# Performance work log

Measured on AMD Instinct MI355X. Metric: run time of the kernel, lower is better.

The kernel has to match this reference:

```python
import jax, jax.numpy as jnp
import numpy as np

D_MODEL = 1024
N_HEADS = 16
NUM_EXPERTS = 8
GATE_HIDDEN = 128
B, T = 4, 2048


def setup_inputs() -> dict:
    key = jax.random.key(0)
    ks = jax.random.split(key, 14)
    s = 0.02
    d, e, gh = D_MODEL, NUM_EXPERTS, GATE_HIDDEN
    return {
        "hidden_states": jax.random.normal(ks[0], (B, T, d), jnp.float32),
        # torch Linear weights are [out_features, in_features]
        "Wq": jax.random.normal(ks[1], (e, d, d), jnp.float32) * s,
        "bq": jax.random.normal(ks[2], (e, d), jnp.float32) * s,
        "Wk": jax.random.normal(ks[3], (e, d, d), jnp.float32) * s,
        "bk": jax.random.normal(ks[4], (e, d), jnp.float32) * s,
        "Wv": jax.random.normal(ks[5], (e, d, d), jnp.float32) * s,
        "bv": jax.random.normal(ks[6], (e, d), jnp.float32) * s,
        "Wg1": jax.random.normal(ks[7], (gh, d), jnp.float32) * s,
        "bg1": jax.random.normal(ks[8], (gh,), jnp.float32) * s,
        "Wg2": jax.random.normal(ks[9], (e, gh), jnp.float32) * s,
        "bg2": jax.random.normal(ks[10], (e,), jnp.float32) * s,
        "Wo": jax.random.normal(ks[11], (d, d), jnp.float32) * s,
        "bo": jax.random.normal(ks[12], (d,), jnp.float32) * s,
    }


def reference(hidden_states, Wq, bq, Wk, bk, Wv, bv, Wg1, bg1, Wg2, bg2, Wo, bo):
    Bb, Tt, C = hidden_states.shape
    H = N_HEADS
    Dh = C // H

    # Per-sample gating over mean-pooled sequence
    pooled = hidden_states.mean(axis=1)                        # [B, C]
    gate_h = jax.nn.relu(pooled @ Wg1.T + bg1)                 # [B, 128]
    gw = jax.nn.softmax(gate_h @ Wg2.T + bg2, axis=-1)         # [B, E]

    # Since gating weights are per-batch scalars, sum_e w_e * (x W_e^T + b_e)
    # == x (sum_e w_e W_e)^T + sum_e w_e b_e  — same math, one GEMM per sample.
    def proj(We, be):
        W_eff = jnp.einsum('be,eoi->boi', gw, We)              # [B, C, C]
        b_eff = gw @ be                                        # [B, C]
        y = jnp.einsum('bti,boi->bto', hidden_states, W_eff) + b_eff[:, None, :]
        return y.reshape(Bb, Tt, H, Dh).transpose(0, 2, 1, 3)  # [B, H, T, Dh]

    q = proj(Wq, bq)
    k = proj(Wk, bk)
    v = proj(Wv, bv)

    scores = jnp.einsum('bhtd,bhsd->bhts', q, k) / (Dh ** 0.5)
    attn = jax.nn.softmax(scores, axis=-1)                     # dropout is inference identity
    out = jnp.einsum('bhts,bhsd->bhtd', attn, v)
    out = out.transpose(0, 2, 1, 3).reshape(Bb, Tt, C)
    return out @ Wo.T + bo
```

## Files before the change

kernel.cpp:

```cpp
#include <hip/hip_runtime.h>

#define B_ 4
#define T_ 2048
#define C_ 1024
#define H_ 16
#define DH_ 64
#define E_ 8
#define GH_ 128

typedef unsigned short bf16_t;
typedef __attribute__((ext_vector_type(8))) __bf16 bf16x8;
typedef __attribute__((ext_vector_type(2))) __bf16 bf16x2;
typedef __attribute__((ext_vector_type(4))) float floatx4;

#if __has_builtin(__builtin_amdgcn_exp2f)
#define EXP2F(x) __builtin_amdgcn_exp2f(x)
#else
#define EXP2F(x) exp2f(x)
#endif

__device__ __forceinline__ bf16_t f2bf(float f) {
  unsigned int u = __builtin_bit_cast(unsigned int, f);
  u += 0x7fffu + ((u >> 16) & 1u);
  return (bf16_t)(u >> 16);
}
__device__ __forceinline__ void async16(const void* g, void* l) {
  __builtin_amdgcn_global_load_lds(
      (const __attribute__((address_space(1))) unsigned int*)g,
      (__attribute__((address_space(3))) unsigned int*)l, 16, 0, 0);
}

__global__ void cvt_kernel(const float* __restrict__ src, bf16_t* __restrict__ dst) {
  int i = (blockIdx.x * 256 + threadIdx.x) * 4;
  float4 v = *(const float4*)(src + i);
  bf16_t o4[4] = {f2bf(v.x), f2bf(v.y), f2bf(v.z), f2bf(v.w)};
  *(uint2*)(dst + i) = *(const uint2*)o4;
}

__global__ void pool_kernel(const float* __restrict__ x, float* __restrict__ partial) {
  int bz = blockIdx.x;
  int b = bz >> 4;
  int r0 = (bz & 15) * 128;
  int t = threadIdx.x;
  float a0 = 0.f, a1 = 0.f, a2 = 0.f, a3 = 0.f;
  const float* xb = x + (size_t)b * T_ * C_ + (size_t)r0 * C_;
  for (int r = 0; r < 128; ++r) {
    const float* row = xb + (size_t)r * C_;
    a0 += row[t]; a1 += row[t + 256]; a2 += row[t + 512]; a3 += row[t + 768];
  }
  float* p = partial + (size_t)bz * C_;
  p[t] = a0; p[t + 256] = a1; p[t + 512] = a2; p[t + 768] = a3;
}

__global__ void gate_kernel(const float* __restrict__ partial,
                            const float* __restrict__ Wg1, const float* __restrict__ bg1,
                            const float* __restrict__ Wg2, const float* __restrict__ bg2,
                            const float* __restrict__ bq, const float* __restrict__ bk,
                            const float* __restrict__ bv,
                            float* __restrict__ gw, float* __restrict__ beff) {
  int b = blockIdx.x;
  int t = threadIdx.x;
  __shared__ float spool[C_];
  __shared__ float sh[GH_];
  __shared__ float sgw[E_];
  for (int i = t; i < C_; i += GH_) {
    float s = 0.f;
    for (int j = 0; j < 16; ++j) s += partial[(size_t)(b * 16 + j) * C_ + i];
    spool[i] = s * (1.0f / T_);
  }
  __syncthreads();
  {
    float acc = 0.f;
    const float* wr = Wg1 + (size_t)t * C_;
    for (int i = 0; i < C_; i += 4) {
      float4 w = *(const float4*)(wr + i);
      acc += spool[i] * w.x + spool[i + 1] * w.y + spool[i + 2] * w.z + spool[i + 3] * w.w;
    }
    acc += bg1[t];
    sh[t] = fmaxf(acc, 0.0f);
  }
  __syncthreads();
  if (t < E_) {
    float acc = 0.f;
    const float* wr = Wg2 + t * GH_;
    for (int j = 0; j < GH_; ++j) acc += sh[j] * wr[j];
    sgw[t] = acc + bg2[t];
  }
  __syncthreads();
  if (t == 0) {
    float mx = sgw[0];
    for (int e = 1; e < E_; ++e) mx = fmaxf(mx, sgw[e]);
    float s = 0.f, ex[E_];
    for (int e = 0; e < E_; ++e) { ex[e] = __expf(sgw[e] - mx); s += ex[e]; }
    float inv = 1.0f / s;
    for (int e = 0; e < E_; ++e) { sgw[e] = ex[e] * inv; gw[b * E_ + e] = sgw[e]; }
  }
  __syncthreads();
  for (int o = t; o < C_; o += GH_) {
    float aq = 0.f, ak = 0.f, av = 0.f;
    #pragma unroll
    for (int e = 0; e < E_; ++e) {
      float w = sgw[e];
      aq += w * bq[e * C_ + o];
      ak += w * bk[e * C_ + o];
      av += w * bv[e * C_ + o];
    }
    beff[(0 * B_ + b) * C_ + o] = aq;
    beff[(1 * B_ + b) * C_ + o] = ak;
    beff[(2 * B_ + b) * C_ + o] = av;
  }
}

__global__ void combine_kernel(const float* __restrict__ Wq, const float* __restrict__ Wk,
                               const float* __restrict__ Wv, const float* __restrict__ gw,
                               bf16_t* __restrict__ Weff) {
  int g = blockIdx.x * 256 + threadIdx.x;
  int ig = (g & 127) * 8;
  int o = (g >> 7) & 1023;
  int p = g >> 17;
  const float* W = (p == 0) ? Wq : (p == 1) ? Wk : Wv;
  const float* src = W + (size_t)o * C_ + ig;
  float acc[B_][8];
  #pragma unroll
  for (int b = 0; b < B_; ++b)
    #pragma unroll
    for (int j = 0; j < 8; ++j) acc[b][j] = 0.f;
  #pragma unroll
  for (int e = 0; e < E_; ++e) {
    float4 lo = *(const float4*)(src + (size_t)e * C_ * C_);
    float4 hi = *(const float4*)(src + (size_t)e * C_ * C_ + 4);
    float w8[8] = {lo.x, lo.y, lo.z, lo.w, hi.x, hi.y, hi.z, hi.w};
    #pragma unroll
    for (int b = 0; b < B_; ++b) {
      float wgt = gw[b * E_ + e];
      #pragma unroll
      for (int j = 0; j < 8; ++j) acc[b][j] += wgt * w8[j];
    }
  }
  #pragma unroll
  for (int b = 0; b < B_; ++b) {
    bf16_t out8[8];
    #pragma unroll
    for (int j = 0; j < 8; ++j) out8[j] = f2bf(acc[b][j]);
    *(uint4*)(Weff + ((size_t)p * B_ + b) * C_ * C_ + (size_t)o * C_ + ig) = *(const uint4*)out8;
  }
}

template <int MODE>
__global__ __launch_bounds__(256) void gemm128(const bf16_t* __restrict__ X,
                                               const bf16_t* __restrict__ W,
                                               const float* __restrict__ bias,
                                               bf16_t* __restrict__ Yb,
                                               float* __restrict__ Yf) {
  if (MODE == 0) {
    int z = blockIdx.z;
    X += (size_t)(z & 3) * (T_ * C_);
    W += (size_t)z * (C_ * C_);
    bias += (size_t)z * C_;
    Yb += (size_t)z * (T_ * C_);
  }
  const int n0 = blockIdx.x * 128;
  const int m0 = blockIdx.y * 128;

  __shared__ __align__(16) bf16_t As[128][64];
  __shared__ __align__(16) bf16_t Bs[128][64];

  const int tid = threadIdx.x;
  const int wave = tid >> 6;
  const int lane = tid & 63;
  const int quad = lane >> 4;
  const int l16 = lane & 15;
  const int wm = (wave & 1) * 64;
  const int wn = (wave >> 1) * 64;

  floatx4 acc[4][4];
  #pragma unroll
  for (int i = 0; i < 4; ++i)
    #pragma unroll
    for (int j = 0; j < 4; ++j) { floatx4 zz = {0.f, 0.f, 0.f, 0.f}; acc[i][j] = zz; }

  const int ar = tid >> 3;
  const int ac = (tid & 7) * 8;
  const bf16_t* Xp = X + (size_t)(m0 + ar) * C_ + ac;
  const bf16_t* Wp = W + (size_t)(n0 + ar) * C_ + ac;

  for (int k0 = 0; k0 < C_; k0 += 64) {
    __syncthreads();
    #pragma unroll
    for (int s = 0; s < 4; ++s) {
      async16(Xp + (size_t)(s * 32) * C_ + k0, &As[ar + s * 32][ac]);
      async16(Wp + (size_t)(s * 32) * C_ + k0, &Bs[ar + s * 32][ac]);
    }
    __syncthreads();
    #pragma unroll
    for (int kk = 0; kk < 64; kk += 32) {
      bf16x8 af[4], bfr[4];
      #pragma unroll
      for (int i = 0; i < 4; ++i) {
        af[i] = *(const bf16x8*)(&As[wm + i * 16 + l16][kk + quad * 8]);
        bfr[i] = *(const bf16x8*)(&Bs[wn + i * 16 + l16][kk + quad * 8]);
      }
      #pragma unroll
      for (int mi = 0; mi < 4; ++mi)
        #pragma unroll
        for (int ni = 0; ni < 4; ++ni)
          acc[mi][ni] = __builtin_amdgcn_mfma_f32_16x16x32_bf16(af[mi], bfr[ni], acc[mi][ni], 0, 0, 0);
    }
  }

  #pragma unroll
  for (int mi = 0; mi < 4; ++mi) {
    #pragma unroll
    for (int ni = 0; ni < 4; ++ni) {
      const int n = n0 + wn + ni * 16 + l16;
      const float bv = bias[n];
      #pragma unroll
      for (int r = 0; r < 4; ++r) {
        const int m = m0 + wm + mi * 16 + quad * 4 + r;
        float v = acc[mi][ni][r] + bv;
        if (MODE == 0) Yb[((size_t)(n >> 6) * T_ + m) * DH_ + (n & 63)] = f2bf(v);
        else           Yf[(size_t)m * C_ + n] = v;
      }
    }
  }
}

__global__ void vtrans_kernel(const bf16_t* __restrict__ qkv, bf16_t* __restrict__ Vt) {
  const int kt = blockIdx.x;
  const int bh = blockIdx.y;
  const int b = bh >> 4, h = bh & 15;
  const bf16_t* src = qkv + (size_t)(8 + b) * T_ * C_ + (size_t)h * T_ * DH_ + (size_t)kt * 64 * DH_;
  __shared__ __align__(16) bf16_t L[64][64];
  const int t = threadIdx.x;
  const int r = t >> 2;
  const int c = (t & 3) * 16;
  const int sw = r & 48;
  *(uint4*)(&L[r][c ^ sw]) = *(const uint4*)(src + (size_t)r * DH_ + c);
  *(uint4*)(&L[r][(c ^ sw) + 8]) = *(const uint4*)(src + (size_t)r * DH_ + c + 8);
  __syncthreads();
  const int sw2 = c & 48;
  bf16_t tmp[16];
  #pragma unroll
  for (int j = 0; j < 16; ++j) tmp[j] = L[c + j][r ^ sw2];
  bf16_t* dst = Vt + (size_t)bh * DH_ * T_ + (size_t)r * T_ + (size_t)kt * 64 + c;
  *(uint4*)(dst) = *(const uint4*)(tmp);
  *(uint4*)(dst + 8) = *(const uint4*)(tmp + 8);
}

__global__ __launch_bounds__(512, 6) void attn_kernel(const bf16_t* __restrict__ qkv,
                                                      const bf16_t* __restrict__ Vt,
                                                      bf16_t* __restrict__ out) {
  const int bh = blockIdx.x;
  const int qt = blockIdx.y;
  const int b = bh >> 4, h = bh & 15;
  const __bf16* Q = (const __bf16*)(qkv + (size_t)b * T_ * C_ + (size_t)h * T_ * DH_);
  const bf16_t* Kp = qkv + (size_t)(4 + b) * T_ * C_ + (size_t)h * T_ * DH_;
  const bf16_t* Vtb = Vt + (size_t)bh * DH_ * T_;

  __shared__ __align__(16) bf16_t Ks[2][4096];
  __shared__ __align__(16) bf16_t Vs[2][4096];
  __shared__ __align__(16) __bf16 Ps[128][72];

  const int tid = threadIdx.x;
  const int wave = tid >> 6;
  const int lane = tid & 63;
  const int quad = lane >> 4;
  const int l16 = lane & 15;

  const float QSC = 0.125f * 1.44269504f;
  bf16x8 qb[2];
  {
    const __bf16* qrow = Q + (size_t)(qt * 128 + wave * 16 + l16) * DH_;
    #pragma unroll
    for (int kc = 0; kc < 2; ++kc) {
      union { bf16x8 v; __bf16 e[8]; } fr;
      #pragma unroll
      for (int j = 0; j < 8; ++j) fr.e[j] = (__bf16)((float)qrow[kc * 32 + quad * 8 + j] * QSC);
      qb[kc] = fr.v;
    }
  }

  int off_[2][4];
  #pragma unroll
  for (int kc = 0; kc < 2; ++kc) {
    #pragma unroll
    for (int i = 0; i < 4; ++i) {
      int row = i * 16 + l16;
      off_[kc][i] = ((row << 3) + (((kc << 2) + quad) ^ (row & 7))) * 8;
    }
  }
  __bf16* prow = &Ps[wave * 16 + l16][0];
  const bf16x8* paptr0 = (const bf16x8*)(prow + 0 * 32 + quad * 8);
  const bf16x8* paptr1 = (const bf16x8*)(prow + 1 * 32 + quad * 8);

  floatx4 oacc[4];
  #pragma unroll
  for (int di = 0; di < 4; ++di) { floatx4 zz = {0.f, 0.f, 0.f, 0.f}; oacc[di] = zz; }
  float lrun = 0.f;

  const int srow = tid >> 3;
  const int schk = (tid & 7) ^ (srow & 7);
  const bf16_t* kg = Kp + (size_t)srow * DH_ + schk * 8;
  const bf16_t* vg = Vtb + (size_t)srow * T_ + schk * 8;

#define STAGE(BUF) do {                                   \
    async16(kg, &Ks[BUF][tid * 8]);                       \
    async16(vg, &Vs[BUF][tid * 8]);                       \
    kg += 64 * DH_;                                       \
    vg += 64;                                             \
  } while (0)

#define WAITV(N) asm volatile("s_waitcnt vmcnt(" #N ")" ::: "memory")
#define BAR() __builtin_amdgcn_s_barrier()

#define COMPUTE(CUR) do {                                                            \
    floatx4 s_[4];                                                                   \
    _Pragma("unroll")                                                                \
    for (int ni = 0; ni < 4; ++ni) { floatx4 zz = {0.f, 0.f, 0.f, 0.f}; s_[ni] = zz; } \
    __builtin_amdgcn_s_setprio(1);                                                   \
    _Pragma("unroll")                                                                \
    for (int kc = 0; kc < 2; ++kc) {                                                 \
      _Pragma("unroll")                                                              \
      for (int ni = 0; ni < 4; ++ni) {                                               \
        bf16x8 ka = *(const bf16x8*)(&Ks[CUR][off_[kc][ni]]);                        \
        s_[ni] = __builtin_amdgcn_mfma_f32_16x16x32_bf16(ka, qb[kc], s_[ni], 0, 0, 0); \
      }                                                                              \
    }                                                                                \
    __builtin_amdgcn_s_setprio(0);                                                   \
    float lsum = 0.f;                                                                \
    _Pragma("unroll")                                                                \
    for (int ni = 0; ni < 4; ++ni) {                                                 \
      float p0 = EXP2F(s_[ni][0]);                                                   \
      float p1 = EXP2F(s_[ni][1]);                                                   \
      float p2 = EXP2F(s_[ni][2]);                                                   \
      float p3 = EXP2F(s_[ni][3]);                                                   \
      lsum += (p0 + p1) + (p2 + p3);                                                 \
      bf16x2 w0 = {(__bf16)p0, (__bf16)p1};                                          \
      bf16x2 w1 = {(__bf16)p2, (__bf16)p3};                                          \
      uint2 pk;                                                                      \
      pk.x = __builtin_bit_cast(unsigned int, w0);                                   \
      pk.y = __builtin_bit_cast(unsigned int, w1);                                   \
      *(uint2*)(prow + ni * 16 + quad * 4) = pk;                                     \
    }                                                                                \
    lsum += __shfl_xor(lsum, 16);                                                    \
    lsum += __shfl_xor(lsum, 32);                                                    \
    lrun += lsum;                                                                    \
    __builtin_amdgcn_s_setprio(1);                                                   \
    _Pragma("unroll")                                                                \
    for (int kc = 0; kc < 2; ++kc) {                                                 \
      bf16x8 pa = *(kc == 0 ? paptr0 : paptr1);                                      \
      _Pragma("unroll")                                                              \
      for (int di = 0; di < 4; ++di) {                                               \
        bf16x8 vb = *(const bf16x8*)(&Vs[CUR][off_[kc][di]]);                        \
        oacc[di] = __builtin_amdgcn_mfma_f32_16x16x32_bf16(pa, vb, oacc[di], 0, 0, 0); \
      }                                                                              \
    }                                                                                \
    __builtin_amdgcn_s_setprio(0);                                                   \
  } while (0)

  STAGE(0);
  #pragma unroll 1
  for (int kt = 0; kt < 30; kt += 2) {
    STAGE(1);
    WAITV(2);
    BAR();
    COMPUTE(0);
    BAR();
    STAGE(0);
    WAITV(2);
    BAR();
    COMPUTE(1);
    BAR();
  }
  STAGE(1);
  WAITV(2);
  BAR();
  COMPUTE(0);
  BAR();
  WAITV(0);
  BAR();
  COMPUTE(1);

#undef STAGE
#undef WAITV
#undef BAR
#undef COMPUTE

  float linv = 1.0f / lrun;
  #pragma unroll
  for (int r = 0; r < 4; ++r) {
    float li = __shfl(linv, quad * 20 + r);
    int m = qt * 128 + wave * 16 + quad * 4 + r;
    #pragma unroll
    for (int di = 0; di < 4; ++di) {
      int d = di * 16 + l16;
      out[(size_t)b * T_ * C_ + (size_t)m * C_ + h * DH_ + d] = f2bf(oacc[di][r] * li);
    }
  }
}

extern "C" void kernel_launch(void* const* d_in, const int* in_sizes, int n_in,
                              void* d_out, int out_size, void* d_ws, size_t ws_size,
                              hipStream_t stream) {
  (void)in_sizes; (void)n_in; (void)out_size; (void)ws_size;
  const float* x   = (const float*)d_in[0];
  const float* Wq  = (const float*)d_in[1];
  const float* bq  = (const float*)d_in[2];
  const float* Wk  = (const float*)d_in[3];
  const float* bk  = (const float*)d_in[4];
  const float* Wv  = (const float*)d_in[5];
  const float* bv  = (const float*)d_in[6];
  const float* Wg1 = (const float*)d_in[7];
  const float* bg1 = (const float*)d_in[8];
  const float* Wg2 = (const float*)d_in[9];
  const float* bg2 = (const float*)d_in[10];
  const float* Wo  = (const float*)d_in[11];
  const float* bo  = (const float*)d_in[12];

  char* ws = (char*)d_ws;
  size_t off = 0;
  auto alloc = [&](size_t bytes) -> void* {
    void* p = ws + off;
    off += (bytes + 255) & ~(size_t)255;
    return p;
  };
  float* partial = (float*)alloc((size_t)B_ * 16 * C_ * 4);
  float* gw      = (float*)alloc((size_t)B_ * E_ * 4);
  float* beff    = (float*)alloc((size_t)3 * B_ * C_ * 4);
  bf16_t* xbf    = (bf16_t*)alloc((size_t)B_ * T_ * C_ * 2);
  bf16_t* Wobf   = (bf16_t*)alloc((size_t)C_ * C_ * 2);
  bf16_t* Weff   = (bf16_t*)alloc((size_t)3 * B_ * C_ * C_ * 2);
  bf16_t* qkv    = (bf16_t*)alloc((size_t)3 * B_ * T_ * C_ * 2);
  bf16_t* attn   = (bf16_t*)alloc((size_t)B_ * T_ * C_ * 2);
  bf16_t* Vt = xbf;

  pool_kernel<<<dim3(B_ * 16), 256, 0, stream>>>(x, partial);
  gate_kernel<<<dim3(B_), GH_, 0, stream>>>(partial, Wg1, bg1, Wg2, bg2,
                                            bq, bk, bv, gw, beff);
  combine_kernel<<<dim3(3 * C_ * (C_ / 8) / 256), 256, 0, stream>>>(Wq, Wk, Wv, gw, Weff);
  cvt_kernel<<<dim3((B_ * T_ * C_) / 1024), 256, 0, stream>>>(x, xbf);
  cvt_kernel<<<dim3((C_ * C_) / 1024), 256, 0, stream>>>(Wo, Wobf);
  gemm128<0><<<dim3(C_ / 128, T_ / 128, 12), 256, 0, stream>>>(xbf, Weff, beff, qkv, nullptr);
  vtrans_kernel<<<dim3(T_ / 64, B_ * H_), 256, 0, stream>>>(qkv, Vt);
  attn_kernel<<<dim3(B_ * H_, T_ / 128), 512, 0, stream>>>(qkv, Vt, attn);
  gemm128<1><<<dim3(C_ / 128, (B_ * T_) / 128, 1), 256, 0, stream>>>(attn, Wobf, bo, nullptr, (float*)d_out);
}
```

Baseline: 453.6 us.

## Switch attention to 32x32 MFMA with register-resident P via permlane swap

The attention kernel moves from 16x16x32 MFMA tiles to 32x32x16 tiles. Each wave now owns 32 query rows and each block 256. The softmax probabilities are rearranged in registers with v_permlane32_swap instead of being written to and read back from shared memory. This removes the Ps LDS buffer and round trip and halves K/V reloads per query row. In exchange it uses more registers, lowers the occupancy hint from 6 to 4 and halves the grid, which may reduce latency hiding.

```diff
diff --git a/kernel.cpp b/kernel.cpp
--- a/kernel.cpp
+++ b/kernel.cpp
@@ -12,6 +12,7 @@
 typedef __attribute__((ext_vector_type(8))) __bf16 bf16x8;
 typedef __attribute__((ext_vector_type(2))) __bf16 bf16x2;
 typedef __attribute__((ext_vector_type(4))) float floatx4;
+typedef __attribute__((ext_vector_type(16))) float floatx16;
 
 #if __has_builtin(__builtin_amdgcn_exp2f)
 #define EXP2F(x) __builtin_amdgcn_exp2f(x)
@@ -247,7 +248,7 @@
   *(uint4*)(dst + 8) = *(const uint4*)(tmp + 8);
 }
 
-__global__ __launch_bounds__(512, 6) void attn_kernel(const bf16_t* __restrict__ qkv,
+__global__ __launch_bounds__(512, 4) void attn_kernel(const bf16_t* __restrict__ qkv,
                                                       const bf16_t* __restrict__ Vt,
                                                       bf16_t* __restrict__ out) {
   const int bh = blockIdx.x;
@@ -259,43 +260,48 @@
 
   __shared__ __align__(16) bf16_t Ks[2][4096];
   __shared__ __align__(16) bf16_t Vs[2][4096];
-  __shared__ __align__(16) __bf16 Ps[128][72];
 
   const int tid = threadIdx.x;
   const int wave = tid >> 6;
   const int lane = tid & 63;
-  const int quad = lane >> 4;
-  const int l16 = lane & 15;
+  const int l31 = lane & 31;
+  const int half = lane >> 5;
 
   const float QSC = 0.125f * 1.44269504f;
-  bf16x8 qb[2];
+  bf16x8 qb[4];
   {
-    const __bf16* qrow = Q + (size_t)(qt * 128 + wave * 16 + l16) * DH_;
-    #pragma unroll
-    for (int kc = 0; kc < 2; ++kc) {
+    const __bf16* qrow = Q + (size_t)(qt * 256 + wave * 32 + l31) * DH_;
+    #pragma unroll
+    for (int kc = 0; kc < 4; ++kc) {
       union { bf16x8 v; __bf16 e[8]; } fr;
       #pragma unroll
-      for (int j = 0; j < 8; ++j) fr.e[j] = (__bf16)((float)qrow[kc * 32 + quad * 8 + j] * QSC);
+      for (int j = 0; j < 8; ++j) fr.e[j] = (__bf16)((float)qrow[kc * 16 + half * 8 + j] * QSC);
       qb[kc] = fr.v;
     }
   }
 
-  int off_[2][4];
-  #pragma unroll
-  for (int kc = 0; kc < 2; ++kc) {
-    #pragma unroll
-    for (int i = 0; i < 4; ++i) {
-      int row = i * 16 + l16;
-      off_[kc][i] = ((row << 3) + (((kc << 2) + quad) ^ (row & 7))) * 8;
-    }
-  }
-  __bf16* prow = &Ps[wave * 16 + l16][0];
-  const bf16x8* paptr0 = (const bf16x8*)(prow + 0 * 32 + quad * 8);
-  const bf16x8* paptr1 = (const bf16x8*)(prow + 1 * 32 + quad * 8);
-
-  floatx4 oacc[4];
-  #pragma unroll
-  for (int di = 0; di < 4; ++di) { floatx4 zz = {0.f, 0.f, 0.f, 0.f}; oacc[di] = zz; }
+  int koff[2][4];
+  int voff[4][2];
+  #pragma unroll
+  for (int kb = 0; kb < 2; ++kb)
+    #pragma unroll
+    for (int kc = 0; kc < 4; ++kc) {
+      int r = kb * 32 + l31;
+      koff[kb][kc] = (r * 8 + ((kc * 2 + half) ^ (r & 7))) * 8;
+    }
+  #pragma unroll
+  for (int c = 0; c < 4; ++c)
+    #pragma unroll
+    for (int db = 0; db < 2; ++db) {
+      int r = db * 32 + l31;
+      voff[c][db] = (r * 8 + ((c * 2 + half) ^ (r & 7))) * 8;
+    }
+
+  floatx16 oacc[2];
+  #pragma unroll
+  for (int db = 0; db < 2; ++db)
+    #pragma unroll
+    for (int i = 0; i < 16; ++i) oacc[db][i] = 0.f;
   float lrun = 0.f;
 
   const int srow = tid >> 3;
@@ -314,48 +320,50 @@
 #define BAR() __builtin_amdgcn_s_barrier()
 
 #define COMPUTE(CUR) do {                                                            \
-    floatx4 s_[4];                                                                   \
     _Pragma("unroll")                                                                \
-    for (int ni = 0; ni < 4; ++ni) { floatx4 zz = {0.f, 0.f, 0.f, 0.f}; s_[ni] = zz; } \
-    __builtin_amdgcn_s_setprio(1);                                                   \
-    _Pragma("unroll")                                                                \
-    for (int kc = 0; kc < 2; ++kc) {                                                 \
+    for (int kb = 0; kb < 2; ++kb) {                                                 \
+      floatx16 s_;                                                                   \
       _Pragma("unroll")                                                              \
-      for (int ni = 0; ni < 4; ++ni) {                                               \
-        bf16x8 ka = *(const bf16x8*)(&Ks[CUR][off_[kc][ni]]);                        \
-        s_[ni] = __builtin_amdgcn_mfma_f32_16x16x32_bf16(ka, qb[kc], s_[ni], 0, 0, 0); \
+      for (int i = 0; i < 16; ++i) s_[i] = 0.f;                                      \
+      __builtin_amdgcn_s_setprio(1);                                                 \
+      _Pragma("unroll")                                                              \
+      for (int kc = 0; kc < 4; ++kc) {                                               \
+        bf16x8 ka = *(const bf16x8*)(&Ks[CUR][koff[kb][kc]]);                        \
+        s_ = __builtin_amdgcn_mfma_f32_32x32x16_bf16(ka, qb[kc], s_, 0, 0, 0);       \
+      }                                                                              \
+      __builtin_amdgcn_s_setprio(0);                                                 \
+      _Pragma("unroll")                                                              \
+      for (int cl = 0; cl < 2; ++cl) {                                               \
+        float e0 = EXP2F(s_[cl * 8 + 0]);                                            \
+        float e1 = EXP2F(s_[cl * 8 + 1]);                                            \
+        float e2 = EXP2F(s_[cl * 8 + 2]);                                            \
+        float e3 = EXP2F(s_[cl * 8 + 3]);                                            \
+        float e4 = EXP2F(s_[cl * 8 + 4]);                                            \
+        float e5 = EXP2F(s_[cl * 8 + 5]);                                            \
+        float e6 = EXP2F(s_[cl * 8 + 6]);                                            \
+        float e7 = EXP2F(s_[cl * 8 + 7]);                                            \
+        lrun += ((e0 + e1) + (e2 + e3)) + ((e4 + e5) + (e6 + e7));                   \
+        bf16x2 w01 = {(__bf16)e0, (__bf16)e1};                                       \
+        bf16x2 w23 = {(__bf16)e2, (__bf16)e3};                                       \
+        bf16x2 w45 = {(__bf16)e4, (__bf16)e5};                                       \
+        bf16x2 w67 = {(__bf16)e6, (__bf16)e7};                                       \
+        unsigned int ua = __builtin_bit_cast(unsigned int, w01);                     \
+        unsigned int ub = __builtin_bit_cast(unsigned int, w23);                     \
+        unsigned int uc = __builtin_bit_cast(unsigned int, w45);                     \
+        unsigned int ud = __builtin_bit_cast(unsigned int, w67);                     \
+        asm("v_permlane32_swap_b32 %0, %1" : "+v"(ua), "+v"(uc));                    \
+        asm("v_permlane32_swap_b32 %0, %1" : "+v"(ub), "+v"(ud));                    \
+        union { unsigned int u[4]; bf16x8 v; } pf;                                   \
+        pf.u[0] = ua; pf.u[1] = ub; pf.u[2] = uc; pf.u[3] = ud;                      \
+        __builtin_amdgcn_s_setprio(1);                                               \
+        _Pragma("unroll")                                                            \
+        for (int db = 0; db < 2; ++db) {                                             \
+          bf16x8 vb = *(const bf16x8*)(&Vs[CUR][voff[kb * 2 + cl][db]]);             \
+          oacc[db] = __builtin_amdgcn_mfma_f32_32x32x16_bf16(pf.v, vb, oacc[db], 0, 0, 0); \
+        }                                                                            \
+        __builtin_amdgcn_s_setprio(0);                                               \
       }                                                                              \
     }                                                                                \
-    __builtin_amdgcn_s_setprio(0);                                                   \
-    float lsum = 0.f;                                                                \
-    _Pragma("unroll")                                                                \
-    for (int ni = 0; ni < 4; ++ni) {                                                 \
-      float p0 = EXP2F(s_[ni][0]);                                                   \
-      float p1 = EXP2F(s_[ni][1]);                                                   \
-      float p2 = EXP2F(s_[ni][2]);                                                   \
-      float p3 = EXP2F(s_[ni][3]);                                                   \
-      lsum += (p0 + p1) + (p2 + p3);                                                 \
-      bf16x2 w0 = {(__bf16)p0, (__bf16)p1};                                          \
-      bf16x2 w1 = {(__bf16)p2, (__bf16)p3};                                          \
-      uint2 pk;                                                                      \
-      pk.x = __builtin_bit_cast(unsigned int, w0);                                   \
-      pk.y = __builtin_bit_cast(unsigned int, w1);                                   \
-      *(uint2*)(prow + ni * 16 + quad * 4) = pk;                                     \
-    }                                                                                \
-    lsum += __shfl_xor(lsum, 16);                                                    \
-    lsum += __shfl_xor(lsum, 32);                                                    \
-    lrun += lsum;                                                                    \
-    __builtin_amdgcn_s_setprio(1);                                                   \
-    _Pragma("unroll")                                                                \
-    for (int kc = 0; kc < 2; ++kc) {                                                 \
-      bf16x8 pa = *(kc == 0 ? paptr0 : paptr1);                                      \
-      _Pragma("unroll")                                                              \
-      for (int di = 0; di < 4; ++di) {                                               \
-        bf16x8 vb = *(const bf16x8*)(&Vs[CUR][off_[kc][di]]);                        \
-        oacc[di] = __builtin_amdgcn_mfma_f32_16x16x32_bf16(pa, vb, oacc[di], 0, 0, 0); \
-      }                                                                              \
-    }                                                                                \
-    __builtin_amdgcn_s_setprio(0);                                                   \
   } while (0)
 
   STAGE(0);
@@ -386,15 +394,17 @@
 #undef BAR
 #undef COMPUTE
 
+  lrun += __shfl_xor(lrun, 32);
   float linv = 1.0f / lrun;
   #pragma unroll
-  for (int r = 0; r < 4; ++r) {
-    float li = __shfl(linv, quad * 20 + r);
-    int m = qt * 128 + wave * 16 + quad * 4 + r;
-    #pragma unroll
-    for (int di = 0; di < 4; ++di) {
-      int d = di * 16 + l16;
-      out[(size_t)b * T_ * C_ + (size_t)m * C_ + h * DH_ + d] = f2bf(oacc[di][r] * li);
+  for (int reg = 0; reg < 16; ++reg) {
+    int mr = (reg & 3) + 8 * (reg >> 2) + 4 * half;
+    float li = __shfl(linv, (lane & 32) | mr);
+    int m = qt * 256 + wave * 32 + mr;
+    #pragma unroll
+    for (int db = 0; db < 2; ++db) {
+      out[(size_t)b * T_ * C_ + (size_t)m * C_ + h * DH_ + db * 32 + l31] =
+          f2bf(oacc[db][reg] * li);
     }
   }
 }
@@ -442,6 +452,6 @@
   cvt_kernel<<<dim3((C_ * C_) / 1024), 256, 0, stream>>>(Wo, Wobf);
   gemm128<0><<<dim3(C_ / 128, T_ / 128, 12), 256, 0, stream>>>(xbf, Weff, beff, qkv, nullptr);
   vtrans_kernel<<<dim3(T_ / 64, B_ * H_), 256, 0, stream>>>(qkv, Vt);
-  attn_kernel<<<dim3(B_ * H_, T_ / 128), 512, 0, stream>>>(qkv, Vt, attn);
+  attn_kernel<<<dim3(B_ * H_, T_ / 256), 512, 0, stream>>>(qkv, Vt, attn);
   gemm128<1><<<dim3(C_ / 128, (B_ * T_) / 128, 1), 256, 0, stream>>>(attn, Wobf, bo, nullptr, (float*)d_out);
 }
```

New measurement: 436.3 us. 3.8% less time.
